# Optimization experiments

Hardware: AMD Instinct MI355X
Metric: run time of the kernel (lower is better)

Reference implementation:

```python
import jax, jax.numpy as jnp
import numpy as np
import math

NUM_HEADS = 4
PH, PW = 8, 8

def setup_inputs() -> dict:
    key = jax.random.key(0)
    ks = jax.random.split(key, 12)
    B, C, H, W = 2, 128, 256, 256
    x = jax.random.normal(ks[0], (B, C, H, W), dtype=jnp.float32)
    mask = jax.random.uniform(ks[1], (B, 1, H, W), dtype=jnp.float32)
    s1 = 1.0 / math.sqrt(C)          # kaiming-ish scale for 1x1 convs
    s3 = 1.0 / math.sqrt(C * 9)      # 3x3 conv
    wq = jax.random.normal(ks[2], (C, C), dtype=jnp.float32) * s1
    bq = jax.random.normal(ks[3], (C,), dtype=jnp.float32) * 0.01
    wk = jax.random.normal(ks[4], (C, C), dtype=jnp.float32) * s1
    bk = jax.random.normal(ks[5], (C,), dtype=jnp.float32) * 0.01
    wv = jax.random.normal(ks[6], (C, C), dtype=jnp.float32) * s1
    bv = jax.random.normal(ks[7], (C,), dtype=jnp.float32) * 0.01
    wo = jax.random.normal(ks[8], (C, C, 3, 3), dtype=jnp.float32) * s3
    bo = jax.random.normal(ks[9], (C,), dtype=jnp.float32) * 0.01
    return {"x": x, "mask": mask, "wq": wq, "bq": bq, "wk": wk, "bk": bk,
            "wv": wv, "bv": bv, "wo": wo, "bo": bo}

def _conv1x1(x, w, b):
    # w: [O, I]; x: [B, C, H, W]
    return jnp.einsum('oc,bchw->bohw', w, x) + b[None, :, None, None]

def _window(t, b, heads, dph, out_h, out_w):
    # [B, C, H, W] -> [B, heads, out_h*out_w, dph*PH*PW]
    t = t.reshape(b, heads, dph, out_h, PH, out_w, PW)
    t = t.transpose(0, 1, 3, 5, 2, 4, 6)
    return t.reshape(b, heads, out_h * out_w, dph * PH * PW)

def reference(x, mask, wq, bq, wk, bk, wv, bv, wo, bo):
    b, c, h, w = x.shape
    heads = NUM_HEADS
    dph = c // heads
    out_h, out_w = h // PH, w // PW
    d = dph * PH * PW

    q = _window(_conv1x1(x, wq, bq), b, heads, dph, out_h, out_w)
    k = _window(_conv1x1(x, wk, bk), b, heads, dph, out_h, out_w)
    v = _window(_conv1x1(x, wv, bv), b, heads, dph, out_h, out_w)

    # NOTE: original torch code calls att.masked_fill(mask, -1e9) without
    # assignment (not in-place), so the mask has no effect on the output.
    att = jnp.einsum('bhqd,bhkd->bhqk', q, k) * (1.0 / math.sqrt(d))
    p = jax.nn.softmax(att, axis=-1)
    y = jnp.einsum('bhqk,bhkd->bhqd', p, v)

    # un-window: [B, heads, S, d] -> [B, C, H, W]
    y = y.reshape(b, heads, out_h, out_w, dph, PH, PW)
    y = y.transpose(0, 1, 4, 2, 5, 3, 6).reshape(b, c, h, w)

    # output: reflect-padded 3x3 conv + LeakyReLU(0.2)
    yp = jnp.pad(y, ((0, 0), (0, 0), (1, 1), (1, 1)), mode='reflect')
    out = jax.lax.conv_general_dilated(
        yp, wo, window_strides=(1, 1), padding='VALID',
        dimension_numbers=('NCHW', 'OIHW', 'NCHW')) + bo[None, :, None, None]
    return jnp.where(out > 0, out, 0.2 * out)
```

## Files before the change

### kernel.cpp

```cpp
#include <hip/hip_runtime.h>
#include <hip/hip_bf16.h>
#include <stdint.h>

typedef unsigned short u16;
typedef __attribute__((ext_vector_type(8))) short bf16x8;
typedef __attribute__((ext_vector_type(4))) short bf16x4;
typedef __attribute__((ext_vector_type(4))) float f32x4;
typedef __attribute__((ext_vector_type(4))) unsigned short u16x4;

__device__ __forceinline__ float bf2f(u16 u) {
  union { unsigned i; float f; } c; c.i = ((unsigned)u) << 16; return c.f;
}
__device__ __forceinline__ u16 f2bf(float f) {
  union { float f; unsigned i; } c; c.f = f;
  unsigned r = c.i + 0x7FFFu + ((c.i >> 16) & 1u);
  return (u16)(r >> 16);
}
__device__ __forceinline__ unsigned cvt_pk(float lo, float hi) {
  unsigned r;
  asm("v_cvt_pk_bf16_f32 %0, %1, %2" : "=v"(r) : "v"(lo), "v"(hi));
  return r;
}
__device__ __forceinline__ void gl2lds16(const u16* g, u16* l) {
  __builtin_amdgcn_global_load_lds(
      (const __attribute__((address_space(1))) unsigned int*)(uintptr_t)g,
      (__attribute__((address_space(3))) unsigned int*)(uintptr_t)l,
      16, 0, 0);
}

__global__ void k_prep(const float* __restrict__ wo, const float* __restrict__ wq,
                       const float* __restrict__ wk, const float* __restrict__ wv,
                       u16* __restrict__ WT, u16* __restrict__ WQKV) {
  int i = blockIdx.x * 256 + threadIdx.x;
  if (i < 9 * 128 * 128) {
    int c = i & 127;
    int o = (i >> 7) & 127;
    int tap = i >> 14;
    WT[i] = f2bf(wo[((o * 128 + c) * 3 + tap / 3) * 3 + tap % 3]);
  } else {
    int j = i - 9 * 128 * 128;
    if (j < 3 * 16384) {
      int sel = j >> 14, rest = j & 16383;
      const float* w = sel == 0 ? wq : (sel == 1 ? wk : wv);
      WQKV[j] = f2bf(w[rest]);
    }
  }
}

__global__ __launch_bounds__(256) void k_qkv(
    const float* __restrict__ x, const u16* __restrict__ WQKV,
    const float* __restrict__ bq, const float* __restrict__ bk,
    const float* __restrict__ bv,
    u16* __restrict__ Q, u16* __restrict__ K, u16* __restrict__ V) {
  const int blk = blockIdx.x;
  const int b = blk >> 9;
  const int t = blk & 511;
  const int th = t & 31, tw = t >> 5;
  const int h0 = th * 8, w0 = tw * 16;
  const int s0 = th * 32 + tw * 2;
  const int tid = threadIdx.x, lane = tid & 63, wid = tid >> 6;
  const int wr = wid >> 1, wc = wid & 1;
  const int g = lane >> 4, l15 = lane & 15;

  __shared__ u16 Ot[128 * 136];

  bf16x8 bfrag[4][4];
  {
    const float* xb = x + (size_t)b * 8388608 + (size_t)(g * 8) * 65536
                        + (h0 + wc * 4) * 256 + w0 + l15;
    #pragma unroll
    for (int ks = 0; ks < 4; ++ks)
      #pragma unroll
      for (int e2 = 0; e2 < 4; ++e2) {
        const float* pa = xb + (size_t)(ks * 32 + e2 * 2) * 65536;
        const float* pb = pa + 65536;
        #pragma unroll
        for (int n = 0; n < 4; ++n)
          ((unsigned*)&bfrag[ks][n])[e2] = cvt_pk(pa[n * 256], pb[n * 256]);
      }
  }

  for (int sel = 0; sel < 3; ++sel) {
    const u16* w = WQKV + sel * 16384;
    const float* bias = sel == 0 ? bq : (sel == 1 ? bk : bv);
    u16* qkv = sel == 0 ? Q : (sel == 1 ? K : V);

    f32x4 acc[4][4] = {};
    #pragma unroll
    for (int ks = 0; ks < 4; ++ks) {
      bf16x8 a[4];
      #pragma unroll
      for (int m = 0; m < 4; ++m) {
        int o = wr * 64 + m * 16 + l15;
        a[m] = *(const bf16x8*)(w + o * 128 + ks * 32 + g * 8);
      }
      #pragma unroll
      for (int m = 0; m < 4; ++m)
        #pragma unroll
        for (int n = 0; n < 4; ++n)
          acc[m][n] = __builtin_amdgcn_mfma_f32_16x16x32_bf16(a[m], bfrag[ks][n], acc[m][n], 0, 0, 0);
    }

    float4 bias4[4];
    #pragma unroll
    for (int m = 0; m < 4; ++m)
      bias4[m] = *(const float4*)&bias[wr * 64 + m * 16 + g * 4];

    __syncthreads();
    #pragma unroll
    for (int m = 0; m < 4; ++m) {
      int o0 = wr * 64 + m * 16 + g * 4;
      #pragma unroll
      for (int n = 0; n < 4; ++n) {
        int p = wc * 64 + n * 16 + l15;
        unsigned r0 = cvt_pk(acc[m][n][0] + bias4[m].x, acc[m][n][1] + bias4[m].y);
        unsigned r1 = cvt_pk(acc[m][n][2] + bias4[m].z, acc[m][n][3] + bias4[m].w);
        unsigned* dp = (unsigned*)&Ot[p * 136 + o0];
        dp[0] = r0; dp[1] = r1;
      }
    }
    __syncthreads();
    #pragma unroll
    for (int it = 0; it < 8; ++it) {
      int head = it >> 1, s2 = it & 1;
      int pixw = tid >> 2;
      int dphc = tid & 3;
      int pl = (pixw >> 3) * 16 + s2 * 8 + (pixw & 7);
      bf16x8 vv = *(const bf16x8*)&Ot[pl * 136 + head * 32 + dphc * 8];
      size_t gaddr = ((size_t)((b * 4 + head) * 1024 + s0 + s2)) * 2048 + pixw * 32 + dphc * 8;
      *(bf16x8*)(qkv + gaddr) = vv;
    }
  }
}

__global__ __launch_bounds__(256) void k_qk(const u16* __restrict__ Q,
                                            const u16* __restrict__ K,
                                            float* __restrict__ ATT) {
  const int bh = blockIdx.x & 7;
  const int tile = blockIdx.x >> 3;
  const int tm = tile & 7, tn = tile >> 3;
  const int row0 = tm * 128, col0 = tn * 128;
  const int tid = threadIdx.x, lane = tid & 63, wid = tid >> 6;
  const int wr = wid >> 1, wc = wid & 1;
  __shared__ u16 As[128 * 32];
  __shared__ u16 Bs[128 * 32];
  const u16* Ab = Q + (size_t)bh * 1024 * 2048 + (size_t)row0 * 2048;
  const u16* Bb = K + (size_t)bh * 1024 * 2048 + (size_t)col0 * 2048;
  f32x4 acc[4][4] = {};
  const int lr = lane >> 2, lc = lane & 3;
  const int scs = lc ^ ((lr >> 1) & 3);
  const int rsw = ((lane & 15) >> 1) & 3;

  for (int k0 = 0; k0 < 2048; k0 += 32) {
    __syncthreads();
    const u16* s0 = Ab + (size_t)(wid * 16 + lr) * 2048 + k0 + scs * 8;
    gl2lds16(s0, &As[wid * 512]);
    gl2lds16(s0 + (size_t)64 * 2048, &As[2048 + wid * 512]);
    const u16* s1 = Bb + (size_t)(wid * 16 + lr) * 2048 + k0 + scs * 8;
    gl2lds16(s1, &Bs[wid * 512]);
    gl2lds16(s1 + (size_t)64 * 2048, &Bs[2048 + wid * 512]);
    asm volatile("s_waitcnt vmcnt(0)" ::: "memory");
    __syncthreads();
    bf16x8 a[4], bb[4];
    const int g = lane >> 4;
    const int chp = (g ^ rsw) * 8;
    #pragma unroll
    for (int m = 0; m < 4; ++m)
      a[m] = *(const bf16x8*)&As[(wr * 64 + m * 16 + (lane & 15)) * 32 + chp];
    #pragma unroll
    for (int n = 0; n < 4; ++n)
      bb[n] = *(const bf16x8*)&Bs[(wc * 64 + n * 16 + (lane & 15)) * 32 + chp];
    #pragma unroll
    for (int m = 0; m < 4; ++m)
      #pragma unroll
      for (int n = 0; n < 4; ++n)
        acc[m][n] = __builtin_amdgcn_mfma_f32_16x16x32_bf16(a[m], bb[n], acc[m][n], 0, 0, 0);
  }
  const float scale = 0.02209708691207961f;
  float* out = ATT + (size_t)bh * 1024 * 1024;
  #pragma unroll
  for (int m = 0; m < 4; ++m) {
    int r = row0 + wr * 64 + m * 16 + ((lane >> 4) << 2);
    #pragma unroll
    for (int n = 0; n < 4; ++n) {
      int cc = col0 + wc * 64 + n * 16 + (lane & 15);
      #pragma unroll
      for (int j = 0; j < 4; ++j)
        out[(size_t)(r + j) * 1024 + cc] = acc[m][n][j] * scale;
    }
  }
}

__global__ __launch_bounds__(256) void k_vt(const u16* __restrict__ V,
                                            u16* __restrict__ VT) {
  const int bh = blockIdx.y;
  const int ts = blockIdx.x & 7, td = blockIdx.x >> 3;
  const int s0 = ts * 128, d0 = td * 128;
  const int tid = threadIdx.x;
  __shared__ u16 T[128 * 128];
  const u16* Vb = V + (size_t)bh * 1024 * 2048 + (size_t)s0 * 2048 + d0;

  #pragma unroll
  for (int pass = 0; pass < 8; ++pass) {
    int r = pass * 16 + (tid >> 4);
    int c8 = (tid & 15) * 8;
    union { uint4 u; u16 e[8]; } d;
    d.u = *(const uint4*)(Vb + (size_t)r * 2048 + c8);
    int chunk = (r >> 3) ^ ((c8 >> 3) & 15);
    u16* dst = &T[0];
    #pragma unroll
    for (int e = 0; e < 8; ++e)
      dst[(c8 + e) * 128 + chunk * 8 + (r & 7)] = d.e[e];
  }
  __syncthreads();
  u16* VTb = VT + (size_t)bh * 2048 * 1024 + (size_t)d0 * 1024 + s0;
  #pragma unroll
  for (int pass = 0; pass < 8; ++pass) {
    int rd = pass * 16 + (tid >> 4);
    int c8 = (tid & 15) * 8;
    int chunk = (c8 >> 3) ^ ((rd >> 3) & 15);
    bf16x8 v = *(const bf16x8*)&T[rd * 128 + chunk * 8];
    *(bf16x8*)(VTb + (size_t)rd * 1024 + c8) = v;
  }
}

__global__ __launch_bounds__(256) void k_softmax(const float* __restrict__ ATT,
                                                 u16* __restrict__ P) {
  const int row = blockIdx.x;
  const float* a = ATT + (size_t)row * 1024;
  const int tid = threadIdx.x;
  float4 v = *(const float4*)(a + tid * 4);
  float mx = fmaxf(fmaxf(v.x, v.y), fmaxf(v.z, v.w));
  #pragma unroll
  for (int off = 32; off; off >>= 1) mx = fmaxf(mx, __shfl_xor(mx, off, 64));
  __shared__ float red[8];
  if ((tid & 63) == 0) red[tid >> 6] = mx;
  __syncthreads();
  mx = fmaxf(fmaxf(red[0], red[1]), fmaxf(red[2], red[3]));
  float e0 = __expf(v.x - mx), e1 = __expf(v.y - mx);
  float e2 = __expf(v.z - mx), e3 = __expf(v.w - mx);
  float s = e0 + e1 + e2 + e3;
  #pragma unroll
  for (int off = 32; off; off >>= 1) s += __shfl_xor(s, off, 64);
  if ((tid & 63) == 0) red[4 + (tid >> 6)] = s;
  __syncthreads();
  s = red[4] + red[5] + red[6] + red[7];
  float inv = 1.0f / s;
  u16x4 o = { f2bf(e0 * inv), f2bf(e1 * inv), f2bf(e2 * inv), f2bf(e3 * inv) };
  *(u16x4*)(P + (size_t)row * 1024 + tid * 4) = o;
}

__global__ __launch_bounds__(256) void k_pv(const u16* __restrict__ P,
                                            const u16* __restrict__ VT,
                                            u16* __restrict__ Yn) {
  const int bh = blockIdx.x & 7;
  const int tile = blockIdx.x >> 3;
  const int tm = tile & 7, tn = tile >> 3;
  const int row0 = tm * 128, col0 = tn * 128;
  const int tid = threadIdx.x, lane = tid & 63, wid = tid >> 6;
  const int wr = wid >> 1, wc = wid & 1;
  __shared__ __align__(16) u16 smem[17408];
  u16* As = smem;
  u16* Bs = smem + 4096;
  u16* Ot = smem;
  const u16* Pb = P + (size_t)bh * 1024 * 1024 + (size_t)row0 * 1024;
  const u16* VTb = VT + (size_t)bh * 2048 * 1024 + (size_t)col0 * 1024;
  f32x4 acc[4][4] = {};
  const int lr = lane >> 2, lc = lane & 3;
  const int scs = lc ^ ((lr >> 1) & 3);
  const int rsw = ((lane & 15) >> 1) & 3;

  for (int k0 = 0; k0 < 1024; k0 += 32) {
    __syncthreads();
    const u16* s0 = Pb + (size_t)(wid * 16 + lr) * 1024 + k0 + scs * 8;
    gl2lds16(s0, &As[wid * 512]);
    gl2lds16(s0 + (size_t)64 * 1024, &As[2048 + wid * 512]);
    const u16* s1 = VTb + (size_t)(wid * 16 + lr) * 1024 + k0 + scs * 8;
    gl2lds16(s1, &Bs[wid * 512]);
    gl2lds16(s1 + (size_t)64 * 1024, &Bs[2048 + wid * 512]);
    asm volatile("s_waitcnt vmcnt(0)" ::: "memory");
    __syncthreads();
    bf16x8 a[4], bb[4];
    const int g = lane >> 4;
    const int chp = (g ^ rsw) * 8;
    #pragma unroll
    for (int m = 0; m < 4; ++m)
      a[m] = *(const bf16x8*)&As[(wr * 64 + m * 16 + (lane & 15)) * 32 + chp];
    #pragma unroll
    for (int n = 0; n < 4; ++n)
      bb[n] = *(const bf16x8*)&Bs[(wc * 64 + n * 16 + (lane & 15)) * 32 + chp];
    #pragma unroll
    for (int m = 0; m < 4; ++m)
      #pragma unroll
      for (int n = 0; n < 4; ++n)
        acc[m][n] = __builtin_amdgcn_mfma_f32_16x16x32_bf16(a[m], bb[n], acc[m][n], 0, 0, 0);
  }

  __syncthreads();
  #pragma unroll
  for (int m = 0; m < 4; ++m) {
    int r0 = wr * 64 + m * 16 + ((lane >> 4) << 2);
    #pragma unroll
    for (int n = 0; n < 4; ++n) {
      int dv = wc * 64 + n * 16 + (lane & 15);
      #pragma unroll
      for (int j = 0; j < 4; ++j)
        Ot[(r0 + j) * 136 + dv] = f2bf(acc[m][n][j]);
    }
  }
  __syncthreads();
  const int b = bh >> 2, head = bh & 3;
  const int pixw0 = tn * 4;
  #pragma unroll
  for (int it = 0; it < 8; ++it) {
    int ci = it * 256 + tid;
    int sl = ci >> 4;
    int pxl = (ci >> 2) & 3;
    int dc = ci & 3;
    bf16x8 vv = *(const bf16x8*)&Ot[sl * 136 + pxl * 32 + dc * 8];
    int s = row0 + sl, oh = s >> 5, ow = s & 31;
    int pixw = pixw0 + pxl, ph = pixw >> 3, pw = pixw & 7;
    int h = oh * 8 + ph, w2 = ow * 8 + pw;
    size_t gaddr = (((size_t)(b * 256 + h) * 256) + w2) * 128 + head * 32 + dc * 8;
    *(bf16x8*)(Yn + gaddr) = vv;
  }
}

__global__ __launch_bounds__(512, 2) void k_conv(const u16* __restrict__ Yn,
                                                 const u16* __restrict__ WT,
                                                 const float* __restrict__ bo,
                                                 float* __restrict__ out) {
  const int wgid = blockIdx.x;
  const int r7 = wgid & 7;
  const int b = (r7 >> 2) & 1;
  const int w0 = ((r7 >> 1) & 1) * 128;
  const int h0 = ((r7 & 1) * 32 + (wgid >> 3)) * 4;
  const int tid = threadIdx.x, lane = tid & 63, wid = tid >> 6;
  const int wo_ = wid & 1;
  const int wh = wid >> 1;
  const int g = lane >> 4, l15 = lane & 15;
  __shared__ u16 S[6][136 * 64];
  __shared__ u16 WTl[2][8192];
  f32x4 acc[4][8] = {};

  auto stageS = [&](int chalf) {
    for (int g5 = wid; g5 < 102; g5 += 8) {
      int rowi = g5 / 17, grp = g5 % 17;
      int rg = grp * 8 + (lane >> 3);
      int chunk = lane & 7;
      int row = h0 + rowi - 1;
      row = row < 0 ? 1 : (row > 255 ? 254 : row);
      int wsrc = w0 - 1 + rg;
      wsrc = wsrc < 0 ? 1 : (wsrc > 255 ? 254 : wsrc);
      const u16* src = Yn + ((size_t)(b * 256 + row) * 256 + wsrc) * 128 + chalf * 64
                         + ((chunk ^ (rg & 7)) * 8);
      gl2lds16(src, &S[rowi][grp * 512]);
    }
  };
  auto stageWT = [&](int chalf, int tap, int nb) {
    #pragma unroll
    for (int r2 = 0; r2 < 2; ++r2) {
      int g5 = wid + r2 * 8;
      int orow = g5 * 8 + (lane >> 3);
      int csrc = (lane & 7) ^ (lane >> 3);
      const u16* src = WT + ((size_t)tap * 128 + orow) * 128 + chalf * 64 + csrc * 8;
      gl2lds16(src, &WTl[nb][g5 * 512]);
    }
  };

  int buf = 0;
  stageS(0);
  stageWT(0, 0, 0);
  asm volatile("s_waitcnt vmcnt(0)" ::: "memory");
  __syncthreads();

  #pragma unroll
  for (int chalf = 0; chalf < 2; ++chalf) {
    if (chalf) {
      __syncthreads();
      stageS(1);
      stageWT(1, 0, buf ^ 1);
      asm volatile("s_waitcnt vmcnt(0)" ::: "memory");
      __syncthreads();
      buf ^= 1;
    }
    #pragma unroll
    for (int ky = 0; ky < 3; ++ky) {
      #pragma unroll
      for (int kx = 0; kx < 3; ++kx) {
        const int tap = ky * 3 + kx;
        const bool hasNext = (tap < 8);
        if (hasNext) stageWT(chalf, tap + 1, buf ^ 1);
        bf16x8 areg[2][4];
        #pragma unroll
        for (int ckh = 0; ckh < 2; ++ckh)
          #pragma unroll
          for (int m = 0; m < 4; ++m) {
            int o = wo_ * 64 + m * 16 + l15;
            int cc2 = ((ckh << 2) + g) ^ (o & 7);
            areg[ckh][m] = *(const bf16x8*)&WTl[buf][o * 64 + cc2 * 8];
          }
        #pragma unroll
        for (int ckh = 0; ckh < 2; ++ckh) {
          #pragma unroll
          for (int nh = 0; nh < 2; ++nh) {
            bf16x8 bb[4];
            #pragma unroll
            for (int n4 = 0; n4 < 4; ++n4) {
              int p = (nh * 4 + n4) * 16 + l15 + kx;
              int chunk = ((ckh << 2) + g) ^ (p & 7);
              bb[n4] = *(const bf16x8*)&S[wh + ky][p * 64 + chunk * 8];
            }
            #pragma unroll
            for (int m = 0; m < 4; ++m)
              #pragma unroll
              for (int n4 = 0; n4 < 4; ++n4)
                acc[m][nh * 4 + n4] = __builtin_amdgcn_mfma_f32_16x16x32_bf16(
                    areg[ckh][m], bb[n4], acc[m][nh * 4 + n4], 0, 0, 0);
          }
        }
        if (hasNext) {
          asm volatile("s_waitcnt vmcnt(0)" ::: "memory");
          __syncthreads();
          buf ^= 1;
        }
      }
    }
  }
  #pragma unroll
  for (int m = 0; m < 4; ++m) {
    int o0 = wo_ * 64 + m * 16 + (g << 2);
    #pragma unroll
    for (int n = 0; n < 8; ++n) {
      int p = n * 16 + l15;
      #pragma unroll
      for (int j = 0; j < 4; ++j) {
        int o = o0 + j;
        float v = acc[m][n][j] + bo[o];
        v = v > 0.f ? v : 0.2f * v;
        out[(((size_t)b * 128 + o) << 16) + ((h0 + wh) << 8) + w0 + p] = v;
      }
    }
  }
}

extern "C" void kernel_launch(void* const* d_in, const int* in_sizes, int n_in,
                              void* d_out, int out_size, void* d_ws, size_t ws_size,
                              hipStream_t stream) {
  const float* x  = (const float*)d_in[0];
  const float* wq = (const float*)d_in[2];
  const float* bq = (const float*)d_in[3];
  const float* wk = (const float*)d_in[4];
  const float* bk = (const float*)d_in[5];
  const float* wv = (const float*)d_in[6];
  const float* bv = (const float*)d_in[7];
  const float* wo = (const float*)d_in[8];
  const float* bo = (const float*)d_in[9];

  char* ws = (char*)d_ws;
  u16*   WT   = (u16*)(ws);
  u16*   WQKV = (u16*)(ws + (size_t)(512 << 10));
  u16*   Q   = (u16*)(ws + (size_t)(1  << 20));
  u16*   K   = (u16*)(ws + (size_t)(33 << 20));
  u16*   V   = (u16*)(ws + (size_t)(65 << 20));
  float* ATT = (float*)(ws + (size_t)(97 << 20));
  u16*   P   = (u16*)(ws + (size_t)(129 << 20));
  u16*   Yn  = (u16*)(ws + (size_t)(145 << 20));
  u16*   VT  = Q;
  float* outp = (float*)d_out;

  k_prep<<<768, 256, 0, stream>>>(wo, wq, wk, wv, WT, WQKV);
  k_qkv<<<1024, 256, 0, stream>>>(x, WQKV, bq, bk, bv, Q, K, V);
  k_qk<<<512, 256, 0, stream>>>(Q, K, ATT);
  k_vt<<<dim3(128, 8), 256, 0, stream>>>(V, VT);
  k_softmax<<<8192, 256, 0, stream>>>(ATT, P);
  k_pv<<<1024, 256, 0, stream>>>(P, VT, Yn);
  k_conv<<<256, 512, 0, stream>>>(Yn, WT, bo, outp);
}
```

Measured before the change: 214.4 us.

## Double-buffer LDS staging in QK and PV GEMMs and merge V transpose launch

The QK and PV GEMM loops now use two LDS buffers, so the global-to-LDS load of the next K-slice is issued before the MFMAs on the current slice, hiding load latency behind compute. The V transpose is folded into the QK launch as extra blocks, which removes one kernel launch and lets the two run concurrently. Because transpose blocks now run at the same time as QK blocks still reading Q, VT moves to its own workspace region instead of aliasing Q. LDS use per block doubles for the GEMMs, which may reduce occupancy.

```diff
diff --git a/kernel.cpp b/kernel.cpp
--- a/kernel.cpp
+++ b/kernel.cpp
@@ -133,94 +133,107 @@
   }
 }
 
-__global__ __launch_bounds__(256) void k_qk(const u16* __restrict__ Q,
-                                            const u16* __restrict__ K,
-                                            float* __restrict__ ATT) {
-  const int bh = blockIdx.x & 7;
-  const int tile = blockIdx.x >> 3;
-  const int tm = tile & 7, tn = tile >> 3;
-  const int row0 = tm * 128, col0 = tn * 128;
+__global__ __launch_bounds__(256) void k_qkvt(const u16* __restrict__ Q,
+                                              const u16* __restrict__ K,
+                                              float* __restrict__ ATT,
+                                              const u16* __restrict__ V,
+                                              u16* __restrict__ VT) {
+  __shared__ __align__(16) u16 smem[16384];
   const int tid = threadIdx.x, lane = tid & 63, wid = tid >> 6;
-  const int wr = wid >> 1, wc = wid & 1;
-  __shared__ u16 As[128 * 32];
-  __shared__ u16 Bs[128 * 32];
-  const u16* Ab = Q + (size_t)bh * 1024 * 2048 + (size_t)row0 * 2048;
-  const u16* Bb = K + (size_t)bh * 1024 * 2048 + (size_t)col0 * 2048;
-  f32x4 acc[4][4] = {};
-  const int lr = lane >> 2, lc = lane & 3;
-  const int scs = lc ^ ((lr >> 1) & 3);
-  const int rsw = ((lane & 15) >> 1) & 3;
-
-  for (int k0 = 0; k0 < 2048; k0 += 32) {
-    __syncthreads();
-    const u16* s0 = Ab + (size_t)(wid * 16 + lr) * 2048 + k0 + scs * 8;
-    gl2lds16(s0, &As[wid * 512]);
-    gl2lds16(s0 + (size_t)64 * 2048, &As[2048 + wid * 512]);
-    const u16* s1 = Bb + (size_t)(wid * 16 + lr) * 2048 + k0 + scs * 8;
-    gl2lds16(s1, &Bs[wid * 512]);
-    gl2lds16(s1 + (size_t)64 * 2048, &Bs[2048 + wid * 512]);
+
+  if (blockIdx.x < 512) {
+    const int bh = blockIdx.x & 7;
+    const int tile = blockIdx.x >> 3;
+    const int tm = tile & 7, tn = tile >> 3;
+    const int row0 = tm * 128, col0 = tn * 128;
+    const int wr = wid >> 1, wc = wid & 1;
+    const u16* Ab = Q + (size_t)bh * 1024 * 2048 + (size_t)row0 * 2048;
+    const u16* Bb = K + (size_t)bh * 1024 * 2048 + (size_t)col0 * 2048;
+    f32x4 acc[4][4] = {};
+    const int lr = lane >> 2, lc = lane & 3;
+    const int scs = lc ^ ((lr >> 1) & 3);
+    const int rsw = ((lane & 15) >> 1) & 3;
+
+    auto stage = [&](int k0, int bf) {
+      u16* As = smem + bf * 8192;
+      u16* Bs = smem + 4096 + bf * 8192;
+      const u16* s0 = Ab + (size_t)(wid * 16 + lr) * 2048 + k0 + scs * 8;
+      gl2lds16(s0, &As[wid * 512]);
+      gl2lds16(s0 + (size_t)64 * 2048, &As[2048 + wid * 512]);
+      const u16* s1 = Bb + (size_t)(wid * 16 + lr) * 2048 + k0 + scs * 8;
+      gl2lds16(s1, &Bs[wid * 512]);
+      gl2lds16(s1 + (size_t)64 * 2048, &Bs[2048 + wid * 512]);
+    };
+
+    stage(0, 0);
     asm volatile("s_waitcnt vmcnt(0)" ::: "memory");
     __syncthreads();
-    bf16x8 a[4], bb[4];
-    const int g = lane >> 4;
-    const int chp = (g ^ rsw) * 8;
-    #pragma unroll
-    for (int m = 0; m < 4; ++m)
-      a[m] = *(const bf16x8*)&As[(wr * 64 + m * 16 + (lane & 15)) * 32 + chp];
-    #pragma unroll
-    for (int n = 0; n < 4; ++n)
-      bb[n] = *(const bf16x8*)&Bs[(wc * 64 + n * 16 + (lane & 15)) * 32 + chp];
-    #pragma unroll
-    for (int m = 0; m < 4; ++m)
+    int cur = 0;
+    for (int k0 = 0; k0 < 2048; k0 += 32) {
+      if (k0 + 32 < 2048) stage(k0 + 32, cur ^ 1);
+      const u16* As = smem + cur * 8192;
+      const u16* Bs = smem + 4096 + cur * 8192;
+      bf16x8 a[4], bb[4];
+      const int g = lane >> 4;
+      const int chp = (g ^ rsw) * 8;
+      #pragma unroll
+      for (int m = 0; m < 4; ++m)
+        a[m] = *(const bf16x8*)&As[(wr * 64 + m * 16 + (lane & 15)) * 32 + chp];
       #pragma unroll
       for (int n = 0; n < 4; ++n)
-        acc[m][n] = __builtin_amdgcn_mfma_f32_16x16x32_bf16(a[m], bb[n], acc[m][n], 0, 0, 0);
-  }
-  const float scale = 0.02209708691207961f;
-  float* out = ATT + (size_t)bh * 1024 * 1024;
-  #pragma unroll
-  for (int m = 0; m < 4; ++m) {
-    int r = row0 + wr * 64 + m * 16 + ((lane >> 4) << 2);
-    #pragma unroll
-    for (int n = 0; n < 4; ++n) {
-      int cc = col0 + wc * 64 + n * 16 + (lane & 15);
-      #pragma unroll
-      for (int j = 0; j < 4; ++j)
-        out[(size_t)(r + j) * 1024 + cc] = acc[m][n][j] * scale;
-    }
-  }
-}
-
-__global__ __launch_bounds__(256) void k_vt(const u16* __restrict__ V,
-                                            u16* __restrict__ VT) {
-  const int bh = blockIdx.y;
-  const int ts = blockIdx.x & 7, td = blockIdx.x >> 3;
-  const int s0 = ts * 128, d0 = td * 128;
-  const int tid = threadIdx.x;
-  __shared__ u16 T[128 * 128];
-  const u16* Vb = V + (size_t)bh * 1024 * 2048 + (size_t)s0 * 2048 + d0;
-
-  #pragma unroll
-  for (int pass = 0; pass < 8; ++pass) {
-    int r = pass * 16 + (tid >> 4);
-    int c8 = (tid & 15) * 8;
-    union { uint4 u; u16 e[8]; } d;
-    d.u = *(const uint4*)(Vb + (size_t)r * 2048 + c8);
-    int chunk = (r >> 3) ^ ((c8 >> 3) & 15);
-    u16* dst = &T[0];
-    #pragma unroll
-    for (int e = 0; e < 8; ++e)
-      dst[(c8 + e) * 128 + chunk * 8 + (r & 7)] = d.e[e];
-  }
-  __syncthreads();
-  u16* VTb = VT + (size_t)bh * 2048 * 1024 + (size_t)d0 * 1024 + s0;
-  #pragma unroll
-  for (int pass = 0; pass < 8; ++pass) {
-    int rd = pass * 16 + (tid >> 4);
-    int c8 = (tid & 15) * 8;
-    int chunk = (c8 >> 3) ^ ((rd >> 3) & 15);
-    bf16x8 v = *(const bf16x8*)&T[rd * 128 + chunk * 8];
-    *(bf16x8*)(VTb + (size_t)rd * 1024 + c8) = v;
+        bb[n] = *(const bf16x8*)&Bs[(wc * 64 + n * 16 + (lane & 15)) * 32 + chp];
+      #pragma unroll
+      for (int m = 0; m < 4; ++m)
+        #pragma unroll
+        for (int n = 0; n < 4; ++n)
+          acc[m][n] = __builtin_amdgcn_mfma_f32_16x16x32_bf16(a[m], bb[n], acc[m][n], 0, 0, 0);
+      asm volatile("s_waitcnt vmcnt(0)" ::: "memory");
+      __syncthreads();
+      cur ^= 1;
+    }
+    const float scale = 0.02209708691207961f;
+    float* out = ATT + (size_t)bh * 1024 * 1024;
+    #pragma unroll
+    for (int m = 0; m < 4; ++m) {
+      int r = row0 + wr * 64 + m * 16 + ((lane >> 4) << 2);
+      #pragma unroll
+      for (int n = 0; n < 4; ++n) {
+        int cc = col0 + wc * 64 + n * 16 + (lane & 15);
+        #pragma unroll
+        for (int j = 0; j < 4; ++j)
+          out[(size_t)(r + j) * 1024 + cc] = acc[m][n][j] * scale;
+      }
+    }
+  } else {
+    const int idx = blockIdx.x - 512;
+    const int bh = idx & 7;
+    const int t2 = idx >> 3;
+    const int ts = t2 & 7, td = t2 >> 3;
+    const int s0 = ts * 128, d0 = td * 128;
+    u16* T = smem;
+    const u16* Vb = V + (size_t)bh * 1024 * 2048 + (size_t)s0 * 2048 + d0;
+
+    #pragma unroll
+    for (int pass = 0; pass < 8; ++pass) {
+      int r = pass * 16 + (tid >> 4);
+      int c8 = (tid & 15) * 8;
+      union { uint4 u; u16 e[8]; } d;
+      d.u = *(const uint4*)(Vb + (size_t)r * 2048 + c8);
+      int chunk = (r >> 3) ^ ((c8 >> 3) & 15);
+      #pragma unroll
+      for (int e = 0; e < 8; ++e)
+        T[(c8 + e) * 128 + chunk * 8 + (r & 7)] = d.e[e];
+    }
+    __syncthreads();
+    u16* VTb = VT + (size_t)bh * 2048 * 1024 + (size_t)d0 * 1024 + s0;
+    #pragma unroll
+    for (int pass = 0; pass < 8; ++pass) {
+      int rd = pass * 16 + (tid >> 4);
+      int c8 = (tid & 15) * 8;
+      int chunk = (c8 >> 3) ^ ((rd >> 3) & 15);
+      bf16x8 v = *(const bf16x8*)&T[rd * 128 + chunk * 8];
+      *(bf16x8*)(VTb + (size_t)rd * 1024 + c8) = v;
+    }
   }
 }
 
@@ -260,8 +273,6 @@
   const int tid = threadIdx.x, lane = tid & 63, wid = tid >> 6;
   const int wr = wid >> 1, wc = wid & 1;
   __shared__ __align__(16) u16 smem[17408];
-  u16* As = smem;
-  u16* Bs = smem + 4096;
   u16* Ot = smem;
   const u16* Pb = P + (size_t)bh * 1024 * 1024 + (size_t)row0 * 1024;
   const u16* VTb = VT + (size_t)bh * 2048 * 1024 + (size_t)col0 * 1024;
@@ -270,16 +281,25 @@
   const int scs = lc ^ ((lr >> 1) & 3);
   const int rsw = ((lane & 15) >> 1) & 3;
 
-  for (int k0 = 0; k0 < 1024; k0 += 32) {
-    __syncthreads();
+  auto stage = [&](int k0, int bf) {
+    u16* As = smem + bf * 8192;
+    u16* Bs = smem + 4096 + bf * 8192;
     const u16* s0 = Pb + (size_t)(wid * 16 + lr) * 1024 + k0 + scs * 8;
     gl2lds16(s0, &As[wid * 512]);
     gl2lds16(s0 + (size_t)64 * 1024, &As[2048 + wid * 512]);
     const u16* s1 = VTb + (size_t)(wid * 16 + lr) * 1024 + k0 + scs * 8;
     gl2lds16(s1, &Bs[wid * 512]);
     gl2lds16(s1 + (size_t)64 * 1024, &Bs[2048 + wid * 512]);
-    asm volatile("s_waitcnt vmcnt(0)" ::: "memory");
-    __syncthreads();
+  };
+
+  stage(0, 0);
+  asm volatile("s_waitcnt vmcnt(0)" ::: "memory");
+  __syncthreads();
+  int cur = 0;
+  for (int k0 = 0; k0 < 1024; k0 += 32) {
+    if (k0 + 32 < 1024) stage(k0 + 32, cur ^ 1);
+    const u16* As = smem + cur * 8192;
+    const u16* Bs = smem + 4096 + cur * 8192;
     bf16x8 a[4], bb[4];
     const int g = lane >> 4;
     const int chp = (g ^ rsw) * 8;
@@ -294,9 +314,11 @@
       #pragma unroll
       for (int n = 0; n < 4; ++n)
         acc[m][n] = __builtin_amdgcn_mfma_f32_16x16x32_bf16(a[m], bb[n], acc[m][n], 0, 0, 0);
-  }
-
-  __syncthreads();
+    asm volatile("s_waitcnt vmcnt(0)" ::: "memory");
+    __syncthreads();
+    cur ^= 1;
+  }
+
   #pragma unroll
   for (int m = 0; m < 4; ++m) {
     int r0 = wr * 64 + m * 16 + ((lane >> 4) << 2);
@@ -466,13 +488,12 @@
   float* ATT = (float*)(ws + (size_t)(97 << 20));
   u16*   P   = (u16*)(ws + (size_t)(129 << 20));
   u16*   Yn  = (u16*)(ws + (size_t)(145 << 20));
-  u16*   VT  = Q;
+  u16*   VT  = (u16*)(ws + (size_t)(177 << 20));
   float* outp = (float*)d_out;
 
   k_prep<<<768, 256, 0, stream>>>(wo, wq, wk, wv, WT, WQKV);
   k_qkv<<<1024, 256, 0, stream>>>(x, WQKV, bq, bk, bv, Q, K, V);
-  k_qk<<<512, 256, 0, stream>>>(Q, K, ATT);
-  k_vt<<<dim3(128, 8), 256, 0, stream>>>(V, VT);
+  k_qkvt<<<1536, 256, 0, stream>>>(Q, K, ATT, V, VT);
   k_softmax<<<8192, 256, 0, stream>>>(ATT, P);
   k_pv<<<1024, 256, 0, stream>>>(P, VT, Yn);
   k_conv<<<256, 512, 0, stream>>>(Yn, WT, bo, outp);
```

Measured after the change: 212.9 us. About the same (-0.7%).
